# Performance work log

Hardware: AMD Instinct MI355X
Metric: run time of the kernel (lower is better)

Reference implementation:

```python
import jax, jax.numpy as jnp
import numpy as np

B, T, D, H = 8192, 2048, 2, 2


def setup_inputs() -> dict:
    key = jax.random.key(0)
    ks = jax.random.split(key, 7)
    return {
        "x": jax.random.normal(ks[0], (B, T, D), dtype=jnp.float32),
        "h0": jax.random.normal(ks[1], (B, H), dtype=jnp.float32),
        "c0": jax.random.normal(ks[2], (B, H), dtype=jnp.float32),
        "w_ih": jax.random.normal(ks[3], (4 * H, D), dtype=jnp.float32),
        "w_hh": jax.random.normal(ks[4], (4 * H, H), dtype=jnp.float32),
        "b_ih": jax.random.normal(ks[5], (4 * H,), dtype=jnp.float32),
        "b_hh": jax.random.normal(ks[6], (4 * H,), dtype=jnp.float32),
    }


def reference(x, h0, c0, w_ih, w_hh, b_ih, b_hh):
    # Precompute input projections for all timesteps in one GEMM: (T, B, 4H)
    xg = jnp.einsum("btd,gd->tbg", x, w_ih) + b_ih

    def step(carry, xt_g):
        h, c = carry
        gates = xt_g + h @ w_hh.T + b_hh  # (B, 4H)
        i, f, g, o = jnp.split(gates, 4, axis=-1)  # torch lstm_cell gate order: i,f,g,o
        c = jax.nn.sigmoid(f) * c + jax.nn.sigmoid(i) * jnp.tanh(g)
        h = jax.nn.sigmoid(o) * jnp.tanh(c)
        return (h, c), None

    (h, c), _ = jax.lax.scan(step, (h0, c0), xg)
    return c
```

## Files before the change

### kernel.cpp

```cpp
#include <hip/hip_runtime.h>


#define LOG2E 1.4426950408889634f

template <int CTRL>
__device__ __forceinline__ float qdpp(float v) {
    int i = __builtin_bit_cast(int, v);
    i = __builtin_amdgcn_update_dpp(0, i, CTRL, 0xF, 0xF, true);
    return __builtin_bit_cast(float, i);
}
template <int CTRL, int BANK>
__device__ __forceinline__ float mdpp(float old, float v) {
    int i = __builtin_amdgcn_update_dpp(__builtin_bit_cast(int, old),
                                        __builtin_bit_cast(int, v),
                                        CTRL, 0xF, BANK, false);
    return __builtin_bit_cast(float, i);
}
#define DPP_MIRROR8 0x141
#define DPP_SWAP2   0x4E
#define DPP_COLSWP  0xB1
#define DPP_ZB_OWN0 0xEE
#define DPP_ZB_OWN1 0x44
#define DPP_ZB_OTH0 0xBB
#define DPP_ZB_OTH1 0x11

__global__ __launch_bounds__(64, 1) void lstm_oct_nh_kernel(
    const float* __restrict__ x,
    const float* __restrict__ h0,
    const float* __restrict__ c0,
    const float* __restrict__ w_ih,
    const float* __restrict__ w_hh,
    const float* __restrict__ b_ih,
    const float* __restrict__ b_hh,
    float* __restrict__ out,
    int B, int T)
{
    const int tid = blockIdx.x * blockDim.x + threadIdx.x;
    const int e = tid >> 3;
    const int q = tid & 7;
    if (e >= B) return;

    const int r = (q < 4) ? q : 11 - q;
    const bool isTanh = (q >= 6);
    const bool sel45  = (q == 4) || (q == 5);
    const bool selMid = (q >= 2) && (q <= 5);
    const int col = (q & 1) ^ ((q >> 2) & 1);

    const float a = isTanh ? (2.0f * LOG2E) : (-LOG2E);
    const float m = isTanh ? (-4.0f * LOG2E) : 1.0f;
    const float d = isTanh ? (2.0f * LOG2E) : 0.0f;

    const float wx0 = w_ih[2 * r] * a, wx1 = w_ih[2 * r + 1] * a;
    const float bias = (b_ih[r] + b_hh[r]) * a;
    const float AwhOwn = w_hh[2 * r + col] * a;
    const float AwhOth = w_hh[2 * r + (1 - col)] * a;
    const float Awh2Own = -2.0f * AwhOwn;
    const float Awh2Oth = -2.0f * AwhOth;

    float r2 = fmaf(-0.5f, h0[2 * e + col], 0.5f);
    float cs = c0[2 * e + col] * (2.0f * LOG2E);
    float V2Own = Awh2Own;
    float V2Oth = Awh2Oth;
    float biasW = bias + AwhOwn + AwhOth;

    const int NI = T >> 1;
    const float4* __restrict__ xp =
        reinterpret_cast<const float4*>(x) + (size_t)e * NI;

    auto step = [&](float x0, float x1) {
        float r2o = qdpp<DPP_COLSWP>(r2);
        float axW = fmaf(wx1, x1, fmaf(wx0, x0, biasW));
        float g   = fmaf(V2Oth, r2o, fmaf(V2Own, r2, axW));
        float n   = fmaf(m, __builtin_amdgcn_rcpf(1.0f + __builtin_amdgcn_exp2f(g)), d);
        float mv  = qdpp<DPP_MIRROR8>(n);
        float X = sel45 ? mv : n;
        float Y = selMid ? cs : mv;
        float p = X * Y;
        float ps = qdpp<DPP_SWAP2>(p);
        cs = p + ps;
        float Ep  = __builtin_amdgcn_exp2f(p);
        float Eps = qdpp<DPP_SWAP2>(Ep);
        r2 = __builtin_amdgcn_rcpf(fmaf(Ep, Eps, 1.0f));
        float zbOwn = mdpp<DPP_ZB_OWN0, 0x5>(mv, mv);
        zbOwn = mdpp<DPP_ZB_OWN1, 0xA>(zbOwn, n);
        float zbOth = mdpp<DPP_ZB_OTH0, 0x5>(mv, mv);
        zbOth = mdpp<DPP_ZB_OTH1, 0xA>(zbOth, n);
        V2Own = Awh2Own * zbOwn;
        V2Oth = Awh2Oth * zbOth;
        biasW = fmaf(AwhOwn, zbOwn, fmaf(AwhOth, zbOth, bias));
    };

    constexpr int BV = 8;
    float4 A[BV], Bb[BV];

    auto loadbuf = [&](float4* buf, int batch) {
#pragma unroll
        for (int j = 0; j < BV; ++j) buf[j] = xp[batch * BV + j];
    };
    auto consume = [&](const float4* buf) {
#pragma unroll
        for (int j = 0; j < BV; ++j) {
            step(buf[j].x, buf[j].y);
            step(buf[j].z, buf[j].w);
        }
    };

    const int nb = NI / BV;
    int bi = 0;
    if (nb >= 2) {
        loadbuf(A, 0);
        loadbuf(Bb, 1);
        for (bi = 0; bi + 1 < nb; bi += 2) {
            consume(A);
            if (bi + 2 < nb) loadbuf(A, bi + 2);
            consume(Bb);
            if (bi + 3 < nb) loadbuf(Bb, bi + 3);
        }
        if (bi < nb) { consume(A); ++bi; }
    }
    for (int i = bi * BV; i < NI; ++i) {
        float4 v = xp[i];
        step(v.x, v.y);
        step(v.z, v.w);
    }

    if (q < 2) out[2 * e + q] = cs * (0.5f / LOG2E);
}

extern "C" void kernel_launch(void* const* d_in, const int* in_sizes, int n_in,
                              void* d_out, int out_size, void* d_ws, size_t ws_size,
                              hipStream_t stream) {
    const float* x    = (const float*)d_in[0];
    const float* h0   = (const float*)d_in[1];
    const float* c0   = (const float*)d_in[2];
    const float* w_ih = (const float*)d_in[3];
    const float* w_hh = (const float*)d_in[4];
    const float* b_ih = (const float*)d_in[5];
    const float* b_hh = (const float*)d_in[6];
    float* out = (float*)d_out;

    const int B = in_sizes[1] / 2;
    const int T = in_sizes[0] / (B * 2);

    const int threads = B * 8;
    dim3 block(64);
    dim3 grid((threads + 63) / 64);
    hipLaunchKernelGGL(lstm_oct_nh_kernel, grid, block, 0, stream,
                       x, h0, c0, w_ih, w_hh, b_ih, b_hh, out, B, T);
}
```

Measured before the change: 324.7 us.

## Fold next-step input projection into recurrence carry, derive zbOth via one DPP swap

The input projection for the next timestep (w_ih·x + bias) is now computed at the end of each step and folded into a single carried value `hw`. The start of the next step therefore only has to do the two recurrent FMAs before the exp, which shortens the serial dependency chain per timestep. The batch loops, prologue and tail are reshaped to pass each next x pair one step ahead. The 'other column' gate term now comes from a single column-swap DPP of zbOwn instead of two masked DPP moves. The catch is more complex boundary handling, plus one extra projection computed with zero inputs at the very end.

```diff
diff --git a/kernel.cpp b/kernel.cpp
--- a/kernel.cpp
+++ b/kernel.cpp
@@ -21,8 +21,6 @@
 #define DPP_COLSWP  0xB1
 #define DPP_ZB_OWN0 0xEE
 #define DPP_ZB_OWN1 0x44
-#define DPP_ZB_OTH0 0xBB
-#define DPP_ZB_OTH1 0x11
 
 __global__ __launch_bounds__(64, 1) void lstm_oct_nh_kernel(
     const float* __restrict__ x,
@@ -61,16 +59,15 @@
     float cs = c0[2 * e + col] * (2.0f * LOG2E);
     float V2Own = Awh2Own;
     float V2Oth = Awh2Oth;
-    float biasW = bias + AwhOwn + AwhOth;
+    float hw = 0.0f;
 
     const int NI = T >> 1;
     const float4* __restrict__ xp =
         reinterpret_cast<const float4*>(x) + (size_t)e * NI;
 
-    auto step = [&](float x0, float x1) {
+    auto step = [&](float x0n, float x1n) {
         float r2o = qdpp<DPP_COLSWP>(r2);
-        float axW = fmaf(wx1, x1, fmaf(wx0, x0, biasW));
-        float g   = fmaf(V2Oth, r2o, fmaf(V2Own, r2, axW));
+        float g   = fmaf(V2Oth, r2o, fmaf(V2Own, r2, hw));
         float n   = fmaf(m, __builtin_amdgcn_rcpf(1.0f + __builtin_amdgcn_exp2f(g)), d);
         float mv  = qdpp<DPP_MIRROR8>(n);
         float X = sel45 ? mv : n;
@@ -81,13 +78,13 @@
         float Ep  = __builtin_amdgcn_exp2f(p);
         float Eps = qdpp<DPP_SWAP2>(Ep);
         r2 = __builtin_amdgcn_rcpf(fmaf(Ep, Eps, 1.0f));
+        float xb = fmaf(wx1, x1n, fmaf(wx0, x0n, bias));
         float zbOwn = mdpp<DPP_ZB_OWN0, 0x5>(mv, mv);
         zbOwn = mdpp<DPP_ZB_OWN1, 0xA>(zbOwn, n);
-        float zbOth = mdpp<DPP_ZB_OTH0, 0x5>(mv, mv);
-        zbOth = mdpp<DPP_ZB_OTH1, 0xA>(zbOth, n);
+        float zbOth = qdpp<DPP_COLSWP>(zbOwn);
         V2Own = Awh2Own * zbOwn;
         V2Oth = Awh2Oth * zbOth;
-        biasW = fmaf(AwhOwn, zbOwn, fmaf(AwhOth, zbOth, bias));
+        hw = fmaf(AwhOth, zbOth, fmaf(AwhOwn, zbOwn, xb));
     };
 
     constexpr int BV = 8;
@@ -97,31 +94,40 @@
 #pragma unroll
         for (int j = 0; j < BV; ++j) buf[j] = xp[batch * BV + j];
     };
-    auto consume = [&](const float4* buf) {
+    auto consume = [&](const float4* buf, float nx0, float nx1) {
 #pragma unroll
         for (int j = 0; j < BV; ++j) {
-            step(buf[j].x, buf[j].y);
             step(buf[j].z, buf[j].w);
+            if (j + 1 < BV) step(buf[j + 1].x, buf[j + 1].y);
+            else            step(nx0, nx1);
         }
     };
 
     const int nb = NI / BV;
     int bi = 0;
+    float tnx0 = 0.0f, tnx1 = 0.0f;
     if (nb >= 2) {
         loadbuf(A, 0);
         loadbuf(Bb, 1);
+        hw = AwhOwn + AwhOth + fmaf(wx1, A[0].y, fmaf(wx0, A[0].x, bias));
+        if (nb * BV < NI) { float4 t0 = xp[nb * BV]; tnx0 = t0.x; tnx1 = t0.y; }
         for (bi = 0; bi + 1 < nb; bi += 2) {
-            consume(A);
-            if (bi + 2 < nb) loadbuf(A, bi + 2);
-            consume(Bb);
+            const bool moreA = bi + 2 < nb;
+            consume(A, Bb[0].x, Bb[0].y);
+            if (moreA) loadbuf(A, bi + 2);
+            consume(Bb, moreA ? A[0].x : tnx0, moreA ? A[0].y : tnx1);
             if (bi + 3 < nb) loadbuf(Bb, bi + 3);
         }
-        if (bi < nb) { consume(A); ++bi; }
+        if (bi < nb) { consume(A, tnx0, tnx1); ++bi; }
+    } else if (NI > 0) {
+        float4 v0 = xp[0];
+        hw = AwhOwn + AwhOth + fmaf(wx1, v0.y, fmaf(wx0, v0.x, bias));
     }
     for (int i = bi * BV; i < NI; ++i) {
         float4 v = xp[i];
-        step(v.x, v.y);
         step(v.z, v.w);
+        if (i + 1 < NI) { float4 w2 = xp[i + 1]; step(w2.x, w2.y); }
+        else            step(0.0f, 0.0f);
     }
 
     if (q < 2) out[2 * e + q] = cs * (0.5f / LOG2E);
```

After: 309.7 us. 1.05x faster.
